# Kernel optimization log

Measured on AMD Instinct MI355X. Metric: run time of the kernel, lower is better.

## Reference

```python
import jax, jax.numpy as jnp
import numpy as np

V, L, D, C = 50000, 512, 300, 128
KS = (3, 4, 5)
B = 64


def setup_inputs() -> dict:
    key = jax.random.key(0)
    ks = jax.random.split(key, 12)
    inp = {
        "x": jax.random.randint(ks[0], (B, L), 0, V),
        "embed_w": jax.random.normal(ks[1], (V, D), jnp.float32) * 0.1,
        "conv_w": jax.random.normal(ks[2], (C, D), jnp.float32) * 0.05,
        "conv_b": jax.random.normal(ks[3], (C,), jnp.float32) * 0.05,
        "fc3_w": jax.random.normal(ks[4], (L - 3,), jnp.float32) * 0.04,
        "fc3_b": jax.random.normal(ks[5], (1,), jnp.float32) * 0.04,
        "fc4_w": jax.random.normal(ks[6], (L - 4,), jnp.float32) * 0.04,
        "fc4_b": jax.random.normal(ks[7], (1,), jnp.float32) * 0.04,
        "fc5_w": jax.random.normal(ks[8], (L - 5,), jnp.float32) * 0.04,
        "fc5_b": jax.random.normal(ks[9], (1,), jnp.float32) * 0.04,
        "fc_w": jax.random.normal(ks[10], (C, C * len(KS)), jnp.float32) * 0.05,
        "fc_b": jax.random.normal(ks[11], (C,), jnp.float32) * 0.05,
    }
    return inp


def reference(x, embed_w, conv_w, conv_b, fc3_w, fc3_b, fc4_w, fc4_b,
              fc5_w, fc5_b, fc_w, fc_b):
    # Embedding lookup: [B, L, D]
    emb = embed_w[x]
    # Exclusive prefix sum over the sequence dim (O(L) sliding sums).
    cs = jnp.concatenate(
        [jnp.zeros_like(emb[:, :1]), jnp.cumsum(emb, axis=1)], axis=1)  # [B, L+1, D]
    fcs = ((fc3_w, fc3_b), (fc4_w, fc4_b), (fc5_w, fc5_b))
    outs = []
    for k, (wk, bk) in zip(KS, fcs):
        # Window i sums tokens i..i+k-1; only L-k windows (range(L-k) in original).
        win = cs[:, k:L] - cs[:, :L - k]                      # [B, L-k, D]
        # conv_sim: dot each window-sum against C label vectors (kernel (1, D)).
        sim = jnp.einsum('bld,cd->bcl', win, conv_w) + conv_b[None, :, None]
        # Dropout is identity in eval; fcs[k]: Linear(L-k, 1) shared across channels.
        outs.append(jnp.einsum('bcl,l->bc', sim, wk) + bk)    # [B, C]
    h = jnp.concatenate(outs, axis=1)                          # [B, C*3]
    return h @ fc_w.T + fc_b                                   # [B, C]
```

## Files before the change

### kernel.cpp

```cpp
#include <hip/hip_runtime.h>
#include <stdint.h>

#define BB 64
#define LL 512
#define DD 300
#define CC 128

#define OFF_GRED  (BB * 32 * 3 * DD)
#define OFF_W2    (OFF_GRED + BB * 3 * DD)
#define OFF_BIAS2 (OFF_W2 + CC * 3 * DD)

__global__ __launch_bounds__(256) void k_gather(
    const int* __restrict__ x, const float* __restrict__ embed,
    const float* __restrict__ conv_w, const float* __restrict__ conv_b,
    const float* __restrict__ w3, const float* __restrict__ b3,
    const float* __restrict__ w4, const float* __restrict__ b4,
    const float* __restrict__ w5, const float* __restrict__ b5,
    const float* __restrict__ fcw, const float* __restrict__ fcb,
    float* __restrict__ Gpart, float* __restrict__ W2,
    float* __restrict__ bias2) {
  const int blk = blockIdx.x;
  const int tid = threadIdx.x;

  if (blk < 1024) {
    const int b = blk >> 4;
    const int tc = blk & 15;
    const int sub = tid >> 7;
    const int stid = tid & 127;

    __shared__ int sx[32];
    __shared__ float su[3][32];

    if (tid < 32) {
      const int t = tc * 32 + tid;
      sx[tid] = x[b * LL + t];
      const float* ws[3] = {w3, w4, w5};
#pragma unroll
      for (int kk = 0; kk < 3; ++kk) {
        const int k = kk + 3;
        int lo = t - k + 1; if (lo < 0) lo = 0;
        int hi = t; const int lim = LL - k - 1; if (hi > lim) hi = lim;
        float s = 0.f;
        for (int l = lo; l <= hi; ++l) s += ws[kk][l];
        su[kk][tid] = s;
      }
    }
    __syncthreads();

    float a0x = 0.f, a0y = 0.f, a1x = 0.f, a1y = 0.f, a2x = 0.f, a2y = 0.f;
    float c0x = 0.f, c0y = 0.f, c1x = 0.f, c1y = 0.f, c2x = 0.f, c2y = 0.f;
    const bool tail = stid < (DD / 2 - 128);

#pragma unroll
    for (int half = 0; half < 2; ++half) {
      const int base = sub * 16 + half * 8;
      float2 v[8], u[8];
#pragma unroll
      for (int i = 0; i < 8; ++i) {
        const float2* rp = (const float2*)(embed + (size_t)sx[base + i] * DD);
        v[i] = rp[stid];
      }
      if (tail) {
#pragma unroll
        for (int i = 0; i < 8; ++i) {
          const float2* rp =
              (const float2*)(embed + (size_t)sx[base + i] * DD);
          u[i] = rp[128 + stid];
        }
      }
#pragma unroll
      for (int i = 0; i < 8; ++i) {
        const int j = base + i;
        const float w0 = su[0][j], w1 = su[1][j], w2 = su[2][j];
        a0x += w0 * v[i].x; a0y += w0 * v[i].y;
        a1x += w1 * v[i].x; a1y += w1 * v[i].y;
        a2x += w2 * v[i].x; a2y += w2 * v[i].y;
        if (tail) {
          c0x += w0 * u[i].x; c0y += w0 * u[i].y;
          c1x += w1 * u[i].x; c1y += w1 * u[i].y;
          c2x += w2 * u[i].x; c2y += w2 * u[i].y;
        }
      }
    }

    const int p = tc * 2 + sub;
    float* Gp = Gpart + (size_t)(b * 32 + p) * (3 * DD);
    const int d0 = 2 * stid;
    Gp[0 * DD + d0] = a0x; Gp[0 * DD + d0 + 1] = a0y;
    Gp[1 * DD + d0] = a1x; Gp[1 * DD + d0 + 1] = a1y;
    Gp[2 * DD + d0] = a2x; Gp[2 * DD + d0 + 1] = a2y;
    if (tail) {
      const int d1 = 2 * (128 + stid);
      Gp[0 * DD + d1] = c0x; Gp[0 * DD + d1 + 1] = c0y;
      Gp[1 * DD + d1] = c1x; Gp[1 * DD + d1 + 1] = c1y;
      Gp[2 * DD + d1] = c2x; Gp[2 * DD + d1 + 1] = c2y;
    }
  } else if (blk < 1504) {
    const int w = (blk - 1024) * 4 + (tid >> 6);
    const int lane = tid & 63;
    const int c = w / 15;
    const int rem = w - c * 15;
    const int kk = rem / 5;
    const int chunk = rem - kk * 5;
    const int d = chunk * 64 + lane;
    if (d < DD) {
      const float* fr = fcw + c * (3 * CC) + kk * CC;
      float acc0 = 0.f, acc1 = 0.f;
#pragma unroll 4
      for (int cp = 0; cp < CC; cp += 2) {
        acc0 += fr[cp] * conv_w[cp * DD + d];
        acc1 += fr[cp + 1] * conv_w[(cp + 1) * DD + d];
      }
      W2[c * (3 * DD) + kk * DD + d] = acc0 + acc1;
    }
  } else {
    const int wid = tid >> 6;
    const int lane = tid & 63;
    const int c = (blk - 1504) * 4 + wid;
    float sk[3];
    const float* ws[3] = {w3, w4, w5};
#pragma unroll
    for (int kk = 0; kk < 3; ++kk) {
      const int len = LL - (kk + 3);
      float s = 0.f;
      for (int l = lane; l < len; l += 64) s += ws[kk][l];
#pragma unroll
      for (int off = 32; off >= 1; off >>= 1) s += __shfl_down(s, off, 64);
      sk[kk] = __shfl(s, 0, 64);
    }
    const float bkv[3] = {b3[0], b4[0], b5[0]};
    float acc = 0.f;
#pragma unroll
    for (int s6 = 0; s6 < 6; ++s6) {
      const int j = s6 * 64 + lane;
      const int kk = j >> 7;
      const int cp = j & 127;
      acc += fcw[c * (3 * CC) + j] * (conv_b[cp] * sk[kk] + bkv[kk]);
    }
#pragma unroll
    for (int off = 32; off >= 1; off >>= 1) acc += __shfl_down(acc, off, 64);
    if (lane == 0) bias2[c] = acc + fcb[c];
  }
}

__global__ __launch_bounds__(256) void k_redout(
    const float* __restrict__ Gpart, const float* __restrict__ W2,
    const float* __restrict__ bias2, float* __restrict__ out) {
  const int b = blockIdx.x >> 2;
  const int cgrp = blockIdx.x & 3;
  const int tid = threadIdx.x;
  __shared__ float gred[3 * DD];

  if (tid < 225) {
    const float4* gp = (const float4*)Gpart + (size_t)b * 32 * 225 + tid;
    float4 s = gp[0];
#pragma unroll
    for (int p = 1; p < 32; ++p) {
      const float4 v = gp[(size_t)p * 225];
      s.x += v.x; s.y += v.y; s.z += v.z; s.w += v.w;
    }
    ((float4*)gred)[tid] = s;
  }
  __syncthreads();

  const int w = tid >> 6;
  const int lane = tid & 63;
  const float2* gr = (const float2*)gred;
#pragma unroll
  for (int pair = 0; pair < 4; ++pair) {
    const int c0 = cgrp * 32 + w * 8 + pair * 2;
    const float2* wr0 = (const float2*)(W2 + c0 * (3 * DD));
    const float2* wr1 = (const float2*)(W2 + (c0 + 1) * (3 * DD));
    float a0 = 0.f, a1 = 0.f;
#pragma unroll
    for (int s = 0; s < 7; ++s) {
      const float2 g = gr[s * 64 + lane];
      const float2 va = wr0[s * 64 + lane];
      const float2 vb = wr1[s * 64 + lane];
      a0 += va.x * g.x + va.y * g.y;
      a1 += vb.x * g.x + vb.y * g.y;
    }
    if (lane < 2) {
      const float2 g = gr[448 + lane];
      const float2 va = wr0[448 + lane];
      const float2 vb = wr1[448 + lane];
      a0 += va.x * g.x + va.y * g.y;
      a1 += vb.x * g.x + vb.y * g.y;
    }
#pragma unroll
    for (int off = 32; off >= 1; off >>= 1) {
      a0 += __shfl_down(a0, off, 64);
      a1 += __shfl_down(a1, off, 64);
    }
    if (lane == 0) {
      out[b * CC + c0] = a0 + bias2[c0];
      out[b * CC + c0 + 1] = a1 + bias2[c0 + 1];
    }
  }
}

extern "C" void kernel_launch(void* const* d_in, const int* in_sizes, int n_in,
                              void* d_out, int out_size, void* d_ws,
                              size_t ws_size, hipStream_t stream) {
  const int* x = (const int*)d_in[0];
  const float* embed = (const float*)d_in[1];
  const float* conv_w = (const float*)d_in[2];
  const float* conv_b = (const float*)d_in[3];
  const float* fc3w = (const float*)d_in[4];
  const float* fc3b = (const float*)d_in[5];
  const float* fc4w = (const float*)d_in[6];
  const float* fc4b = (const float*)d_in[7];
  const float* fc5w = (const float*)d_in[8];
  const float* fc5b = (const float*)d_in[9];
  const float* fcw = (const float*)d_in[10];
  const float* fcb = (const float*)d_in[11];

  float* Gpart = (float*)d_ws;
  float* W2 = (float*)d_ws + OFF_W2;
  float* bias2 = (float*)d_ws + OFF_BIAS2;

  k_gather<<<dim3(1536), dim3(256), 0, stream>>>(
      x, embed, conv_w, conv_b, fc3w, fc3b, fc4w, fc4b, fc5w, fc5b, fcw, fcb,
      Gpart, W2, bias2);
  k_redout<<<dim3(256), dim3(256), 0, stream>>>(Gpart, W2, bias2,
                                                (float*)d_out);
}
```

Baseline: 129.0 us.

## Fuse reduction/output stage into main kernel via last-block atomic counter

Removes the separate reduction/output kernel. Each gather block bumps a per-batch atomic counter, and the last of the 16 blocks for a batch waits for the W2/bias blocks to finish (spin on a done counter), then reduces the partials and writes all 128 outputs. A tiny init kernel zeros the counters. This trades one kernel launch for atomics, a spin-wait, and a serial tail in which only 64 blocks each compute 128 channels. The spin-wait also assumes the W2 blocks get scheduled while gather blocks spin, which risks deadlock or delay.

```diff
diff --git a/kernel.cpp b/kernel.cpp
--- a/kernel.cpp
+++ b/kernel.cpp
@@ -9,8 +9,15 @@
 #define OFF_GRED  (BB * 32 * 3 * DD)
 #define OFF_W2    (OFF_GRED + BB * 3 * DD)
 #define OFF_BIAS2 (OFF_W2 + CC * 3 * DD)
-
-__global__ __launch_bounds__(256) void k_gather(
+#define OFF_CNT   (OFF_BIAS2 + CC)
+#define OFF_WDONE (OFF_CNT + BB)
+#define W2_BLOCKS 512
+
+__global__ __launch_bounds__(256) void k_init(int* __restrict__ cnt) {
+  if (threadIdx.x < BB + 1) cnt[threadIdx.x] = 0;
+}
+
+__global__ __launch_bounds__(256) void k_main(
     const int* __restrict__ x, const float* __restrict__ embed,
     const float* __restrict__ conv_w, const float* __restrict__ conv_b,
     const float* __restrict__ w3, const float* __restrict__ b3,
@@ -18,7 +25,8 @@
     const float* __restrict__ w5, const float* __restrict__ b5,
     const float* __restrict__ fcw, const float* __restrict__ fcb,
     float* __restrict__ Gpart, float* __restrict__ W2,
-    float* __restrict__ bias2) {
+    float* __restrict__ bias2, int* __restrict__ bcount,
+    int* __restrict__ wdone, float* __restrict__ out) {
   const int blk = blockIdx.x;
   const int tid = threadIdx.x;
 
@@ -30,6 +38,8 @@
 
     __shared__ int sx[32];
     __shared__ float su[3][32];
+    __shared__ int lastflag;
+    __shared__ float gred[3 * DD];
 
     if (tid < 32) {
       const int t = tc * 32 + tid;
@@ -94,6 +104,70 @@
       Gp[0 * DD + d1] = c0x; Gp[0 * DD + d1 + 1] = c0y;
       Gp[1 * DD + d1] = c1x; Gp[1 * DD + d1 + 1] = c1y;
       Gp[2 * DD + d1] = c2x; Gp[2 * DD + d1 + 1] = c2y;
+    }
+
+    __threadfence();
+    __syncthreads();
+    if (tid == 0) {
+      const int old = atomicAdd(&bcount[b], 1);
+      lastflag = (old == 15) ? 1 : 0;
+    }
+    __syncthreads();
+    if (!lastflag) return;
+
+    if (tid == 0) {
+      while (atomicAdd(wdone, 0) != W2_BLOCKS) {
+        __builtin_amdgcn_s_sleep(2);
+      }
+    }
+    __syncthreads();
+    __threadfence();
+
+    if (tid < 225) {
+      const float4* gp = (const float4*)Gpart + (size_t)b * 32 * 225 + tid;
+      float4 s = gp[0];
+#pragma unroll
+      for (int q = 1; q < 32; ++q) {
+        const float4 vv = gp[(size_t)q * 225];
+        s.x += vv.x; s.y += vv.y; s.z += vv.z; s.w += vv.w;
+      }
+      ((float4*)gred)[tid] = s;
+    }
+    __syncthreads();
+
+    const int w = tid >> 6;
+    const int lane = tid & 63;
+    const float2* gr = (const float2*)gred;
+#pragma unroll
+    for (int pair = 0; pair < 16; ++pair) {
+      const int ch0 = w * 32 + pair * 2;
+      const float2* wr0 = (const float2*)(W2 + ch0 * (3 * DD));
+      const float2* wr1 = (const float2*)(W2 + (ch0 + 1) * (3 * DD));
+      float g0 = 0.f, g1 = 0.f;
+#pragma unroll
+      for (int s = 0; s < 7; ++s) {
+        const float2 g = gr[s * 64 + lane];
+        const float2 va = wr0[s * 64 + lane];
+        const float2 vb = wr1[s * 64 + lane];
+        g0 += va.x * g.x + va.y * g.y;
+        g1 += vb.x * g.x + vb.y * g.y;
+      }
+      if (lane < 2) {
+        const float2 g = gr[448 + lane];
+        const float2 va = wr0[448 + lane];
+        const float2 vb = wr1[448 + lane];
+        g0 += va.x * g.x + va.y * g.y;
+        g1 += vb.x * g.x + vb.y * g.y;
+      }
+#pragma unroll
+      for (int off = 32; off >= 1; off >>= 1) {
+        g0 += __shfl_down(g0, off, 64);
+        g1 += __shfl_down(g1, off, 64);
+      }
+      if (lane == 0) {
+        out[b * CC + ch0] = g0 + bias2[ch0];
+        out[b * CC + ch0 + 1] = g1 + bias2[ch0 + 1];
+      }
     }
   } else if (blk < 1504) {
     const int w = (blk - 1024) * 4 + (tid >> 6);
@@ -113,6 +187,9 @@
       }
       W2[c * (3 * DD) + kk * DD + d] = acc0 + acc1;
     }
+    __threadfence();
+    __syncthreads();
+    if (tid == 0) atomicAdd(wdone, 1);
   } else {
     const int wid = tid >> 6;
     const int lane = tid & 63;
@@ -140,62 +217,9 @@
 #pragma unroll
     for (int off = 32; off >= 1; off >>= 1) acc += __shfl_down(acc, off, 64);
     if (lane == 0) bias2[c] = acc + fcb[c];
-  }
-}
-
-__global__ __launch_bounds__(256) void k_redout(
-    const float* __restrict__ Gpart, const float* __restrict__ W2,
-    const float* __restrict__ bias2, float* __restrict__ out) {
-  const int b = blockIdx.x >> 2;
-  const int cgrp = blockIdx.x & 3;
-  const int tid = threadIdx.x;
-  __shared__ float gred[3 * DD];
-
-  if (tid < 225) {
-    const float4* gp = (const float4*)Gpart + (size_t)b * 32 * 225 + tid;
-    float4 s = gp[0];
-#pragma unroll
-    for (int p = 1; p < 32; ++p) {
-      const float4 v = gp[(size_t)p * 225];
-      s.x += v.x; s.y += v.y; s.z += v.z; s.w += v.w;
-    }
-    ((float4*)gred)[tid] = s;
-  }
-  __syncthreads();
-
-  const int w = tid >> 6;
-  const int lane = tid & 63;
-  const float2* gr = (const float2*)gred;
-#pragma unroll
-  for (int pair = 0; pair < 4; ++pair) {
-    const int c0 = cgrp * 32 + w * 8 + pair * 2;
-    const float2* wr0 = (const float2*)(W2 + c0 * (3 * DD));
-    const float2* wr1 = (const float2*)(W2 + (c0 + 1) * (3 * DD));
-    float a0 = 0.f, a1 = 0.f;
-#pragma unroll
-    for (int s = 0; s < 7; ++s) {
-      const float2 g = gr[s * 64 + lane];
-      const float2 va = wr0[s * 64 + lane];
-      const float2 vb = wr1[s * 64 + lane];
-      a0 += va.x * g.x + va.y * g.y;
-      a1 += vb.x * g.x + vb.y * g.y;
-    }
-    if (lane < 2) {
-      const float2 g = gr[448 + lane];
-      const float2 va = wr0[448 + lane];
-      const float2 vb = wr1[448 + lane];
-      a0 += va.x * g.x + va.y * g.y;
-      a1 += vb.x * g.x + vb.y * g.y;
-    }
-#pragma unroll
-    for (int off = 32; off >= 1; off >>= 1) {
-      a0 += __shfl_down(a0, off, 64);
-      a1 += __shfl_down(a1, off, 64);
-    }
-    if (lane == 0) {
-      out[b * CC + c0] = a0 + bias2[c0];
-      out[b * CC + c0 + 1] = a1 + bias2[c0 + 1];
-    }
+    __threadfence();
+    __syncthreads();
+    if (tid == 0) atomicAdd(wdone, 1);
   }
 }
 
@@ -218,10 +242,11 @@
   float* Gpart = (float*)d_ws;
   float* W2 = (float*)d_ws + OFF_W2;
   float* bias2 = (float*)d_ws + OFF_BIAS2;
-
-  k_gather<<<dim3(1536), dim3(256), 0, stream>>>(
+  int* bcount = (int*)((float*)d_ws + OFF_CNT);
+  int* wdone = (int*)((float*)d_ws + OFF_WDONE);
+
+  k_init<<<dim3(1), dim3(256), 0, stream>>>(bcount);
+  k_main<<<dim3(1536), dim3(256), 0, stream>>>(
       x, embed, conv_w, conv_b, fc3w, fc3b, fc4w, fc4b, fc5w, fc5b, fcw, fcb,
-      Gpart, W2, bias2);
-  k_redout<<<dim3(256), dim3(256), 0, stream>>>(Gpart, W2, bias2,
-                                                (float*)d_out);
+      Gpart, W2, bias2, bcount, wdone, (float*)d_out);
 }
```

Measured after the change: 344.0 us. +166.7%, slower.

## Split partial-sum reduction and output GEMV into separate wide-grid kernels

Applied to the files above, without the earlier changes.

Replaces the fused reduce-and-output kernel with two kernels. The first uses 16 lanes per float4 output and a shuffle tree to reduce the 32 partials across 900 blocks. The second computes the output dot products with one wavefront per (batch, channel pair) across 1024 blocks. The aim is to remove the serial 32-step reduction that each of 256 blocks repeated four times, and to expose more parallelism. The cost is an extra kernel launch and a global round trip for the reduced buffer.

```diff
diff --git a/kernel.cpp b/kernel.cpp
--- a/kernel.cpp
+++ b/kernel.cpp
@@ -143,59 +143,64 @@
   }
 }
 
-__global__ __launch_bounds__(256) void k_redout(
-    const float* __restrict__ Gpart, const float* __restrict__ W2,
+__global__ __launch_bounds__(256) void k_reduce(
+    const float* __restrict__ Gpart, float* __restrict__ Gred) {
+  const int gid = blockIdx.x * 256 + threadIdx.x;
+  const int o = gid >> 4;
+  const int r = gid & 15;
+  const int b = o / 225;
+  const int q = o - b * 225;
+  const float4* gp =
+      (const float4*)Gpart + (size_t)b * 32 * 225 + (size_t)(2 * r) * 225 + q;
+  const float4 v0 = gp[0];
+  const float4 v1 = gp[225];
+  float4 s;
+  s.x = v0.x + v1.x; s.y = v0.y + v1.y; s.z = v0.z + v1.z; s.w = v0.w + v1.w;
+#pragma unroll
+  for (int off = 1; off <= 8; off <<= 1) {
+    s.x += __shfl_down(s.x, off, 64);
+    s.y += __shfl_down(s.y, off, 64);
+    s.z += __shfl_down(s.z, off, 64);
+    s.w += __shfl_down(s.w, off, 64);
+  }
+  if (r == 0) ((float4*)Gred)[o] = s;
+}
+
+__global__ __launch_bounds__(256) void k_out(
+    const float* __restrict__ Gred, const float* __restrict__ W2,
     const float* __restrict__ bias2, float* __restrict__ out) {
-  const int b = blockIdx.x >> 2;
-  const int cgrp = blockIdx.x & 3;
-  const int tid = threadIdx.x;
-  __shared__ float gred[3 * DD];
-
-  if (tid < 225) {
-    const float4* gp = (const float4*)Gpart + (size_t)b * 32 * 225 + tid;
-    float4 s = gp[0];
-#pragma unroll
-    for (int p = 1; p < 32; ++p) {
-      const float4 v = gp[(size_t)p * 225];
-      s.x += v.x; s.y += v.y; s.z += v.z; s.w += v.w;
-    }
-    ((float4*)gred)[tid] = s;
-  }
-  __syncthreads();
-
-  const int w = tid >> 6;
-  const int lane = tid & 63;
-  const float2* gr = (const float2*)gred;
-#pragma unroll
-  for (int pair = 0; pair < 4; ++pair) {
-    const int c0 = cgrp * 32 + w * 8 + pair * 2;
-    const float2* wr0 = (const float2*)(W2 + c0 * (3 * DD));
-    const float2* wr1 = (const float2*)(W2 + (c0 + 1) * (3 * DD));
-    float a0 = 0.f, a1 = 0.f;
-#pragma unroll
-    for (int s = 0; s < 7; ++s) {
-      const float2 g = gr[s * 64 + lane];
-      const float2 va = wr0[s * 64 + lane];
-      const float2 vb = wr1[s * 64 + lane];
-      a0 += va.x * g.x + va.y * g.y;
-      a1 += vb.x * g.x + vb.y * g.y;
-    }
-    if (lane < 2) {
-      const float2 g = gr[448 + lane];
-      const float2 va = wr0[448 + lane];
-      const float2 vb = wr1[448 + lane];
-      a0 += va.x * g.x + va.y * g.y;
-      a1 += vb.x * g.x + vb.y * g.y;
-    }
-#pragma unroll
-    for (int off = 32; off >= 1; off >>= 1) {
-      a0 += __shfl_down(a0, off, 64);
-      a1 += __shfl_down(a1, off, 64);
-    }
-    if (lane == 0) {
-      out[b * CC + c0] = a0 + bias2[c0];
-      out[b * CC + c0 + 1] = a1 + bias2[c0 + 1];
-    }
+  const int wg = blockIdx.x * 4 + (threadIdx.x >> 6);
+  const int lane = threadIdx.x & 63;
+  const int b = wg >> 6;
+  const int c0 = (wg & 63) * 2;
+
+  const float2* gr = (const float2*)(Gred + b * (3 * DD));
+  const float2* wr0 = (const float2*)(W2 + c0 * (3 * DD));
+  const float2* wr1 = (const float2*)(W2 + (c0 + 1) * (3 * DD));
+  float a0 = 0.f, a1 = 0.f;
+#pragma unroll
+  for (int s = 0; s < 7; ++s) {
+    const float2 g = gr[s * 64 + lane];
+    const float2 va = wr0[s * 64 + lane];
+    const float2 vb = wr1[s * 64 + lane];
+    a0 += va.x * g.x + va.y * g.y;
+    a1 += vb.x * g.x + vb.y * g.y;
+  }
+  if (lane < 2) {
+    const float2 g = gr[448 + lane];
+    const float2 va = wr0[448 + lane];
+    const float2 vb = wr1[448 + lane];
+    a0 += va.x * g.x + va.y * g.y;
+    a1 += vb.x * g.x + vb.y * g.y;
+  }
+#pragma unroll
+  for (int off = 32; off >= 1; off >>= 1) {
+    a0 += __shfl_down(a0, off, 64);
+    a1 += __shfl_down(a1, off, 64);
+  }
+  if (lane == 0) {
+    out[b * CC + c0] = a0 + bias2[c0];
+    out[b * CC + c0 + 1] = a1 + bias2[c0 + 1];
   }
 }
 
@@ -216,12 +221,14 @@
   const float* fcb = (const float*)d_in[11];
 
   float* Gpart = (float*)d_ws;
+  float* Gred = (float*)d_ws + OFF_GRED;
   float* W2 = (float*)d_ws + OFF_W2;
   float* bias2 = (float*)d_ws + OFF_BIAS2;
 
   k_gather<<<dim3(1536), dim3(256), 0, stream>>>(
       x, embed, conv_w, conv_b, fc3w, fc3b, fc4w, fc4b, fc5w, fc5b, fcw, fcb,
       Gpart, W2, bias2);
-  k_redout<<<dim3(256), dim3(256), 0, stream>>>(Gpart, W2, bias2,
-                                                (float*)d_out);
-}
+  k_reduce<<<dim3(900), dim3(256), 0, stream>>>(Gpart, Gred);
+  k_out<<<dim3(1024), dim3(256), 0, stream>>>(Gred, W2, bias2,
+                                              (float*)d_out);
+}
```

Result: no change. 130.0 us (+0.8%).
